# Optimization experiments

Measured on AMD Instinct MI355X. Metric: run time of the kernel, lower is better.

## Reference

```python
import jax, jax.numpy as jnp
import numpy as np

NUM_EMBEDDINGS = 1024
EMBEDDING_DIM = 64
COMMITMENT_COST = 0.25


def setup_inputs() -> dict:
    key = jax.random.key(0)
    k1, k2 = jax.random.split(key)
    inputs = jax.random.normal(k1, (16, EMBEDDING_DIM, 64, 64), dtype=jnp.float32)
    # nn.Embedding weight init: uniform(-1/K, 1/K)
    emb = jax.random.uniform(
        k2, (NUM_EMBEDDINGS, EMBEDDING_DIM), dtype=jnp.float32,
        minval=-1.0 / NUM_EMBEDDINGS, maxval=1.0 / NUM_EMBEDDINGS)
    return {"inputs": inputs, "emb": emb}


def reference(inputs, emb):
    # NCHW -> NHWC
    x = jnp.transpose(inputs, (0, 2, 3, 1))  # [B,H,W,D]
    B, H, W, D = x.shape
    K = emb.shape[0]
    flat = x.reshape(-1, D)  # [N,D]

    # squared L2 distances to every codebook entry: [N,K]
    distances = (jnp.sum(flat * flat, axis=1, keepdims=True)
                 + jnp.sum(emb * emb, axis=1)
                 - 2.0 * jnp.matmul(flat, emb.T))
    idx = jnp.argmin(distances, axis=1)  # [N]
    indices = idx.reshape(B, H, W)[:, None]  # [B,1,H,W]

    # gather == one-hot @ emb, but without the dense matmul
    quantized = emb[idx].reshape(B, H, W, D)

    e_latent_loss = jnp.mean((jax.lax.stop_gradient(quantized) - x) ** 2)
    q_latent_loss = jnp.mean((quantized - jax.lax.stop_gradient(x)) ** 2)
    loss = q_latent_loss + COMMITMENT_COST * e_latent_loss

    # straight-through estimator
    quantized_st = x + jax.lax.stop_gradient(quantized - x)

    # one-hot encodings are part of the module's return contract
    encodings = jax.nn.one_hot(idx, K, dtype=jnp.float32)  # [N,K]
    avg_probs = jnp.mean(encodings, axis=0)
    perplexity = jnp.exp(-jnp.sum(avg_probs * jnp.log(avg_probs + 1e-10)))

    quantized_out = jnp.transpose(quantized_st, (0, 3, 1, 2))  # back to NCHW
    return (loss, quantized_out, perplexity, encodings, indices)
```

## Files before the change

### kernel.cpp

```cpp
#include <hip/hip_runtime.h>

#define NPIX    65536
#define D       64
#define KCODES  1024
#define PIXB    32
#define BLOCK   256
#define XPAD    68
#define CAP     64
#define GFAC    0.036f

#define QUANT_OFF 1
#define PERP_OFF  4194305
#define ENC_OFF   4194306u
#define IDX_OFF   71303170u


typedef float f32x4 __attribute__((ext_vector_type(4)));
typedef short bf16x8 __attribute__((ext_vector_type(8)));

__device__ __forceinline__ unsigned short f2bf(float f) {
    unsigned u = __float_as_uint(f);
    return (unsigned short)((u + 0x7fffu + ((u >> 16) & 1u)) >> 16);
}

__global__ __launch_bounds__(256) void vq_init(const float* __restrict__ emb,
                                               double* __restrict__ loss_sum,
                                               int* __restrict__ counts,
                                               float* __restrict__ se,
                                               int* __restrict__ semax_bits,
                                               unsigned short* __restrict__ ebf) {
    int t = blockIdx.x * 256 + threadIdx.x;
    if (t == 0) *loss_sum = 0.0;
    if (t < KCODES) {
        counts[t] = 0;
        const float* e = emb + (size_t)t * D;
        float r[8];
        #pragma unroll
        for (int j = 0; j < 8; ++j) r[j] = __fmul_rn(e[j], e[j]);
        #pragma unroll
        for (int i = 8; i < D; i += 8)
            #pragma unroll
            for (int j = 0; j < 8; ++j)
                r[j] = __fadd_rn(r[j], __fmul_rn(e[i + j], e[i + j]));
        float X = __fadd_rn(__fadd_rn(r[0], r[1]), __fadd_rn(r[2], r[3]));
        float Y = __fadd_rn(__fadd_rn(r[4], r[5]), __fadd_rn(r[6], r[7]));
        float S = __fadd_rn(X, Y);
        se[t] = S;
        atomicMax(semax_bits, __float_as_int(S));
        #pragma unroll
        for (int j = 0; j < D; ++j) ebf[(t << 6) + j] = f2bf(e[j]);
    }
}

__global__ __launch_bounds__(256) void vq_main(const float* __restrict__ in,
                                               const float* __restrict__ emb,
                                               const float* __restrict__ se,
                                               const int* __restrict__ semax_bits,
                                               const unsigned short* __restrict__ ebf,
                                               float* __restrict__ out,
                                               double* __restrict__ loss_sum,
                                               int* __restrict__ counts) {
    __shared__ float xs[PIXB][XPAD];
    __shared__ float sls[KCODES];
    __shared__ float wmin[4][PIXB];
    __shared__ float gate[PIXB];
    __shared__ float sxs[PIXB];
    __shared__ int   cnt[PIXB];
    __shared__ int   skfin[PIXB];
    __shared__ unsigned short list[PIXB][CAP];

    const int tid  = threadIdx.x;
    const int lane = tid & 63;
    const int wid  = tid >> 6;
    const int n0   = blockIdx.x * PIXB;
    const int b    = n0 >> 12;
    const int s0   = n0 & 4095;

    {
        const float* base = in + ((size_t)b << 18) + s0;
        #pragma unroll
        for (int i = 0; i < 8; ++i) {
            int idx = tid + (i << 8);
            int d   = idx >> 5;
            int px  = idx & 31;
            xs[px][d] = base[((size_t)d << 12) + px];
        }
        #pragma unroll
        for (int i = 0; i < 4; ++i)
            sls[tid + (i << 8)] = se[tid + (i << 8)];
    }
    __syncthreads();

    if (tid < PIXB) {
        cnt[tid] = 0;
        float r[8];
        #pragma unroll
        for (int j = 0; j < 8; ++j) {
            float v = xs[tid][j];
            r[j] = __fmul_rn(v, v);
        }
        #pragma unroll
        for (int i = 8; i < D; i += 8)
            #pragma unroll
            for (int j = 0; j < 8; ++j) {
                float v = xs[tid][i + j];
                r[j] = __fadd_rn(r[j], __fmul_rn(v, v));
            }
        float X = __fadd_rn(__fadd_rn(r[0], r[1]), __fadd_rn(r[2], r[3]));
        float Y = __fadd_rn(__fadd_rn(r[4], r[5]), __fadd_rn(r[6], r[7]));
        sxs[tid] = __fadd_rn(X, Y);
    }

    const int wbase = wid * 256;
    const int arow  = lane & 15;
    const int kgrp  = (lane >> 4) << 3;
    const int rbase = (lane >> 4) << 2;

    bf16x8 af[2][2];
    #pragma unroll
    for (int ks = 0; ks < 2; ++ks)
        #pragma unroll
        for (int pt = 0; pt < 2; ++pt) {
            const float* xp = &xs[pt * 16 + arow][ks * 32 + kgrp];
            bf16x8 v;
            #pragma unroll
            for (int j = 0; j < 8; ++j) v[j] = (short)f2bf(xp[j]);
            af[ks][pt] = v;
        }

    float mreg[2][4];
    #pragma unroll
    for (int pt = 0; pt < 2; ++pt)
        #pragma unroll
        for (int r = 0; r < 4; ++r) mreg[pt][r] = 3.0e38f;

    #pragma unroll
    for (int s2 = 0; s2 < 8; ++s2) {
        const int cbase = wbase + s2 * 32;
        f32x4 acc[2][2];
        #pragma unroll
        for (int pt = 0; pt < 2; ++pt)
            #pragma unroll
            for (int kt = 0; kt < 2; ++kt) acc[pt][kt] = (f32x4){0.f, 0.f, 0.f, 0.f};
        #pragma unroll
        for (int ks = 0; ks < 2; ++ks)
            #pragma unroll
            for (int kt = 0; kt < 2; ++kt) {
                int code = cbase + kt * 16 + arow;
                bf16x8 bf_ = *(const bf16x8*)(ebf + ((size_t)code << 6) + ks * 32 + kgrp);
                #pragma unroll
                for (int pt = 0; pt < 2; ++pt)
                    acc[pt][kt] = __builtin_amdgcn_mfma_f32_16x16x32_bf16(
                        af[ks][pt], bf_, acc[pt][kt], 0, 0, 0);
            }
        #pragma unroll
        for (int pt = 0; pt < 2; ++pt)
            #pragma unroll
            for (int kt = 0; kt < 2; ++kt) {
                int code = cbase + kt * 16 + arow;
                #pragma unroll
                for (int r = 0; r < 4; ++r) {
                    float sv = __fsub_rn(sls[code], __fmul_rn(2.0f, acc[pt][kt][r]));
                    mreg[pt][r] = fminf(mreg[pt][r], sv);
                }
            }
    }
    #pragma unroll
    for (int m = 1; m < 16; m <<= 1)
        #pragma unroll
        for (int pt = 0; pt < 2; ++pt)
            #pragma unroll
            for (int r = 0; r < 4; ++r)
                mreg[pt][r] = fminf(mreg[pt][r], __shfl_xor(mreg[pt][r], m));
    if (arow == 0) {
        #pragma unroll
        for (int pt = 0; pt < 2; ++pt)
            #pragma unroll
            for (int r = 0; r < 4; ++r)
                wmin[wid][pt * 16 + rbase + r] = mreg[pt][r];
    }
    __syncthreads();

    if (tid < PIXB) {
        float gm = wmin[0][tid];
        #pragma unroll
        for (int w = 1; w < 4; ++w) gm = fminf(gm, wmin[w][tid]);
        float semax = __int_as_float(*semax_bits);
        gate[tid] = gm + GFAC * sqrtf(sxs[tid] * semax);
    }
    __syncthreads();

    #pragma unroll
    for (int s2 = 0; s2 < 8; ++s2) {
        const int cbase = wbase + s2 * 32;
        f32x4 acc[2][2];
        #pragma unroll
        for (int pt = 0; pt < 2; ++pt)
            #pragma unroll
            for (int kt = 0; kt < 2; ++kt) acc[pt][kt] = (f32x4){0.f, 0.f, 0.f, 0.f};
        #pragma unroll
        for (int ks = 0; ks < 2; ++ks)
            #pragma unroll
            for (int kt = 0; kt < 2; ++kt) {
                int code = cbase + kt * 16 + arow;
                bf16x8 bf_ = *(const bf16x8*)(ebf + ((size_t)code << 6) + ks * 32 + kgrp);
                #pragma unroll
                for (int pt = 0; pt < 2; ++pt)
                    acc[pt][kt] = __builtin_amdgcn_mfma_f32_16x16x32_bf16(
                        af[ks][pt], bf_, acc[pt][kt], 0, 0, 0);
            }
        #pragma unroll
        for (int pt = 0; pt < 2; ++pt)
            #pragma unroll
            for (int kt = 0; kt < 2; ++kt) {
                int code = cbase + kt * 16 + arow;
                #pragma unroll
                for (int r = 0; r < 4; ++r) {
                    float sv = __fsub_rn(sls[code], __fmul_rn(2.0f, acc[pt][kt][r]));
                    int px = pt * 16 + rbase + r;
                    if (sv <= gate[px]) {
                        int slot = atomicAdd(&cnt[px], 1);
                        if (slot < CAP) list[px][slot] = (unsigned short)code;
                    }
                }
            }
    }
    __syncthreads();

    {
        const int px = tid >> 3, c0 = tid & 7;
        const int cn = cnt[px];
        float bv = 3.0e38f;
        int   bk = 0x7fffffff;
        if (cn > CAP || cn == 0) {
            for (int k = c0; k < KCODES; k += 8) {
                const float* er = emb + ((size_t)k << 6);
                float m = 0.f;
                #pragma unroll
                for (int d = 0; d < D; ++d) m = fmaf(xs[px][d], er[d], m);
                float sv = __fsub_rn(__fadd_rn(sxs[px], sls[k]), __fmul_rn(2.0f, m));
                if (sv < bv || (sv == bv && k < bk)) { bv = sv; bk = k; }
            }
        } else {
            for (int i = c0; i < cn; i += 8) {
                int k = list[px][i];
                const float* er = emb + ((size_t)k << 6);
                float m = 0.f;
                #pragma unroll
                for (int d = 0; d < D; ++d) m = fmaf(xs[px][d], er[d], m);
                float sv = __fsub_rn(__fadd_rn(sxs[px], sls[k]), __fmul_rn(2.0f, m));
                if (sv < bv || (sv == bv && k < bk)) { bv = sv; bk = k; }
            }
        }
        #pragma unroll
        for (int m = 4; m; m >>= 1) {
            float ov = __shfl_xor(bv, m);
            int   ok = __shfl_xor(bk, m);
            if (ov < bv || (ov == bv && ok < bk)) { bv = ov; bk = ok; }
        }
        if (c0 == 0) {
            skfin[px] = bk;
            atomicAdd(&counts[bk], 1);
            out[IDX_OFF + (unsigned)(n0 + px)] = (float)bk;
        }
    }
    __syncthreads();

    {
        float* qbase = out + QUANT_OFF + ((size_t)b << 18) + s0;
        float mse = 0.f;
        #pragma unroll
        for (int i = 0; i < 8; ++i) {
            int idx = tid + (i << 8);
            int d   = idx >> 5;
            int px  = idx & 31;
            float q = emb[((size_t)skfin[px] << 6) + d];
            qbase[((size_t)d << 12) + px] = q;
            float df = q - xs[px][d];
            mse = fmaf(df, df, mse);
        }
        #pragma unroll
        for (int off = 32; off; off >>= 1) mse += __shfl_down(mse, off);
        if (lane == 0) atomicAdd(loss_sum, (double)mse);
    }

    {
        float4* dst4 = (float4*)(out + ENC_OFF + (size_t)n0 * KCODES + 2);
        for (int i = tid; i < 8191; i += BLOCK) {
            int flat = (i << 2) + 2;
            int r0 = flat >> 10;
            int r1 = (flat + 3) >> 10;
            int k0 = skfin[r0];
            int k1 = skfin[r1];
            int c  = flat & 1023;
            float4 v;
            v.x = (c == k0) ? 1.f : 0.f;
            v.y = (c + 1 == k0) ? 1.f : 0.f;
            v.z = (((flat + 2) & 1023) == k1) ? 1.f : 0.f;
            v.w = (((flat + 3) & 1023) == k1) ? 1.f : 0.f;
            dst4[i] = v;
        }
        if (tid == 0) {
            float2* dh = (float2*)(out + ENC_OFF + (size_t)n0 * KCODES);
            int kh = skfin[0];
            float2 h2; h2.x = (kh == 0) ? 1.f : 0.f; h2.y = (kh == 1) ? 1.f : 0.f;
            *dh = h2;
            float2* dt = (float2*)(out + ENC_OFF + (size_t)n0 * KCODES + 32766);
            int kt = skfin[31];
            float2 t2; t2.x = (kt == 1022) ? 1.f : 0.f; t2.y = (kt == 1023) ? 1.f : 0.f;
            *dt = t2;
        }
    }
}

__global__ __launch_bounds__(256) void vq_fin(const double* __restrict__ loss_sum,
                                              const int* __restrict__ counts,
                                              float* __restrict__ out) {
    __shared__ double red[256];
    int t = threadIdx.x;
    double ent = 0.0;
    for (int k = t; k < KCODES; k += 256) {
        double p = (double)counts[k] / 65536.0;
        ent -= p * log(p + 1e-10);
    }
    red[t] = ent;
    __syncthreads();
    for (int o = 128; o; o >>= 1) {
        if (t < o) red[t] += red[t + o];
        __syncthreads();
    }
    if (t == 0) {
        out[PERP_OFF] = (float)exp(red[0]);
        out[0] = (float)(1.25 * (*loss_sum) / 4194304.0);
    }
}

extern "C" void kernel_launch(void* const* d_in, const int* in_sizes, int n_in,
                              void* d_out, int out_size, void* d_ws, size_t ws_size,
                              hipStream_t stream) {
    const float* in  = (const float*)d_in[0];
    const float* emb = (const float*)d_in[1];
    float* out = (float*)d_out;

    double*         loss_sum   = (double*)d_ws;
    int*            counts     = (int*)((char*)d_ws + 8);
    float*          se         = (float*)((char*)d_ws + 4104);
    int*            semax_bits = (int*)((char*)d_ws + 8200);
    unsigned short* ebf        = (unsigned short*)((char*)d_ws + 8320);

    vq_init<<<4, 256, 0, stream>>>(emb, loss_sum, counts, se, semax_bits, ebf);
    vq_main<<<NPIX / PIXB, BLOCK, 0, stream>>>(in, emb, se, semax_bits, ebf,
                                               out, loss_sum, counts);
    vq_fin<<<1, 256, 0, stream>>>(loss_sum, counts, out);
}
```

Baseline: 189.6 us.

## Give each wavefront its own 16 pixels over all codes, removing block barriers

Work is repartitioned so each wave owns 16 pixels and scans the full 1024-code codebook, instead of four waves splitting the codebook across 32 shared pixels. This drops the cross-wave min reduction and the block-wide __syncthreads between the gate, candidate, rescore and output phases, leaving only compiler barriers. Blocks now cover 64 pixels, and the candidate list cap is halved. In exchange, each MFMA B-fragment load from the bf16 codebook is reused by fewer pixel tiles, so codebook traffic per pixel roughly doubles. The smaller cap also makes the full 1024-code fallback scan more likely.

```diff
diff --git a/kernel.cpp b/kernel.cpp
--- a/kernel.cpp
+++ b/kernel.cpp
@@ -3,10 +3,12 @@
 #define NPIX    65536
 #define D       64
 #define KCODES  1024
-#define PIXB    32
+#define PPW     16
+#define WPB     4
+#define PIXB    (PPW*WPB)
 #define BLOCK   256
 #define XPAD    68
-#define CAP     64
+#define CAP     32
 #define GFAC    0.036f
 
 #define QUANT_OFF 1
@@ -60,30 +62,28 @@
                                                float* __restrict__ out,
                                                double* __restrict__ loss_sum,
                                                int* __restrict__ counts) {
-    __shared__ float xs[PIXB][XPAD];
+    __shared__ float xsw[WPB][PPW][XPAD];
     __shared__ float sls[KCODES];
-    __shared__ float wmin[4][PIXB];
-    __shared__ float gate[PIXB];
-    __shared__ float sxs[PIXB];
-    __shared__ int   cnt[PIXB];
-    __shared__ int   skfin[PIXB];
-    __shared__ unsigned short list[PIXB][CAP];
+    __shared__ unsigned short listw[WPB][PPW][CAP];
+    __shared__ int   cntw[WPB][PPW];
+    __shared__ int   skw[WPB][PPW];
+    __shared__ float sxw[WPB][PPW];
 
     const int tid  = threadIdx.x;
     const int lane = tid & 63;
     const int wid  = tid >> 6;
-    const int n0   = blockIdx.x * PIXB;
-    const int b    = n0 >> 12;
-    const int s0   = n0 & 4095;
-
-    {
-        const float* base = in + ((size_t)b << 18) + s0;
-        #pragma unroll
-        for (int i = 0; i < 8; ++i) {
-            int idx = tid + (i << 8);
-            int d   = idx >> 5;
-            int px  = idx & 31;
-            xs[px][d] = base[((size_t)d << 12) + px];
+    const int c0   = lane & 15;
+    const int grp  = lane >> 4;
+    const int n0w  = blockIdx.x * PIXB + wid * PPW;
+    const int b    = n0w >> 12;
+    const int s0w  = n0w & 4095;
+
+    {
+        const float* base = in + ((size_t)b << 18) + s0w;
+        #pragma unroll
+        for (int i = 0; i < 16; ++i) {
+            int d = i * 4 + grp;
+            xsw[wid][c0][d] = base[((size_t)d << 12) + c0];
         }
         #pragma unroll
         for (int i = 0; i < 4; ++i)
@@ -91,192 +91,135 @@
     }
     __syncthreads();
 
-    if (tid < PIXB) {
-        cnt[tid] = 0;
+    if (lane < PPW) {
+        cntw[wid][lane] = 0;
         float r[8];
         #pragma unroll
         for (int j = 0; j < 8; ++j) {
-            float v = xs[tid][j];
+            float v = xsw[wid][lane][j];
             r[j] = __fmul_rn(v, v);
         }
         #pragma unroll
         for (int i = 8; i < D; i += 8)
             #pragma unroll
             for (int j = 0; j < 8; ++j) {
-                float v = xs[tid][i + j];
+                float v = xsw[wid][lane][i + j];
                 r[j] = __fadd_rn(r[j], __fmul_rn(v, v));
             }
         float X = __fadd_rn(__fadd_rn(r[0], r[1]), __fadd_rn(r[2], r[3]));
         float Y = __fadd_rn(__fadd_rn(r[4], r[5]), __fadd_rn(r[6], r[7]));
-        sxs[tid] = __fadd_rn(X, Y);
-    }
-
-    const int wbase = wid * 256;
-    const int arow  = lane & 15;
-    const int kgrp  = (lane >> 4) << 3;
-    const int rbase = (lane >> 4) << 2;
-
-    bf16x8 af[2][2];
+        sxw[wid][lane] = __fadd_rn(X, Y);
+    }
+
+    bf16x8 af[2];
     #pragma unroll
-    for (int ks = 0; ks < 2; ++ks)
-        #pragma unroll
-        for (int pt = 0; pt < 2; ++pt) {
-            const float* xp = &xs[pt * 16 + arow][ks * 32 + kgrp];
-            bf16x8 v;
-            #pragma unroll
-            for (int j = 0; j < 8; ++j) v[j] = (short)f2bf(xp[j]);
-            af[ks][pt] = v;
-        }
-
-    float mreg[2][4];
+    for (int ks = 0; ks < 2; ++ks) {
+        const float* xp = &xsw[wid][c0][ks * 32 + (grp << 3)];
+        bf16x8 v;
+        #pragma unroll
+        for (int j = 0; j < 8; ++j) v[j] = (short)f2bf(xp[j]);
+        af[ks] = v;
+    }
+    const float semax = __int_as_float(*semax_bits);
+
+    float m[4] = {3.0e38f, 3.0e38f, 3.0e38f, 3.0e38f};
+    for (int t = 0; t < 64; ++t) {
+        f32x4 acc = (f32x4){0.f, 0.f, 0.f, 0.f};
+        #pragma unroll
+        for (int ks = 0; ks < 2; ++ks) {
+            bf16x8 bf_ = *(const bf16x8*)(ebf + ((size_t)((t << 4) + c0) << 6)
+                                          + ks * 32 + (grp << 3));
+            acc = __builtin_amdgcn_mfma_f32_16x16x32_bf16(af[ks], bf_, acc, 0, 0, 0);
+        }
+        float sl = sls[(t << 4) + c0];
+        #pragma unroll
+        for (int r = 0; r < 4; ++r) {
+            float sv = __fsub_rn(sl, __fmul_rn(2.0f, acc[r]));
+            m[r] = fminf(m[r], sv);
+        }
+    }
     #pragma unroll
-    for (int pt = 0; pt < 2; ++pt)
-        #pragma unroll
-        for (int r = 0; r < 4; ++r) mreg[pt][r] = 3.0e38f;
-
+    for (int msk = 1; msk < 16; msk <<= 1)
+        #pragma unroll
+        for (int r = 0; r < 4; ++r)
+            m[r] = fminf(m[r], __shfl_xor(m[r], msk));
+
+    float gate[4];
     #pragma unroll
-    for (int s2 = 0; s2 < 8; ++s2) {
-        const int cbase = wbase + s2 * 32;
-        f32x4 acc[2][2];
-        #pragma unroll
-        for (int pt = 0; pt < 2; ++pt)
-            #pragma unroll
-            for (int kt = 0; kt < 2; ++kt) acc[pt][kt] = (f32x4){0.f, 0.f, 0.f, 0.f};
-        #pragma unroll
-        for (int ks = 0; ks < 2; ++ks)
-            #pragma unroll
-            for (int kt = 0; kt < 2; ++kt) {
-                int code = cbase + kt * 16 + arow;
-                bf16x8 bf_ = *(const bf16x8*)(ebf + ((size_t)code << 6) + ks * 32 + kgrp);
-                #pragma unroll
-                for (int pt = 0; pt < 2; ++pt)
-                    acc[pt][kt] = __builtin_amdgcn_mfma_f32_16x16x32_bf16(
-                        af[ks][pt], bf_, acc[pt][kt], 0, 0, 0);
-            }
-        #pragma unroll
-        for (int pt = 0; pt < 2; ++pt)
-            #pragma unroll
-            for (int kt = 0; kt < 2; ++kt) {
-                int code = cbase + kt * 16 + arow;
-                #pragma unroll
-                for (int r = 0; r < 4; ++r) {
-                    float sv = __fsub_rn(sls[code], __fmul_rn(2.0f, acc[pt][kt][r]));
-                    mreg[pt][r] = fminf(mreg[pt][r], sv);
-                }
-            }
-    }
-    #pragma unroll
-    for (int m = 1; m < 16; m <<= 1)
-        #pragma unroll
-        for (int pt = 0; pt < 2; ++pt)
-            #pragma unroll
-            for (int r = 0; r < 4; ++r)
-                mreg[pt][r] = fminf(mreg[pt][r], __shfl_xor(mreg[pt][r], m));
-    if (arow == 0) {
-        #pragma unroll
-        for (int pt = 0; pt < 2; ++pt)
-            #pragma unroll
-            for (int r = 0; r < 4; ++r)
-                wmin[wid][pt * 16 + rbase + r] = mreg[pt][r];
-    }
-    __syncthreads();
-
-    if (tid < PIXB) {
-        float gm = wmin[0][tid];
-        #pragma unroll
-        for (int w = 1; w < 4; ++w) gm = fminf(gm, wmin[w][tid]);
-        float semax = __int_as_float(*semax_bits);
-        gate[tid] = gm + GFAC * sqrtf(sxs[tid] * semax);
-    }
-    __syncthreads();
-
-    #pragma unroll
-    for (int s2 = 0; s2 < 8; ++s2) {
-        const int cbase = wbase + s2 * 32;
-        f32x4 acc[2][2];
-        #pragma unroll
-        for (int pt = 0; pt < 2; ++pt)
-            #pragma unroll
-            for (int kt = 0; kt < 2; ++kt) acc[pt][kt] = (f32x4){0.f, 0.f, 0.f, 0.f};
-        #pragma unroll
-        for (int ks = 0; ks < 2; ++ks)
-            #pragma unroll
-            for (int kt = 0; kt < 2; ++kt) {
-                int code = cbase + kt * 16 + arow;
-                bf16x8 bf_ = *(const bf16x8*)(ebf + ((size_t)code << 6) + ks * 32 + kgrp);
-                #pragma unroll
-                for (int pt = 0; pt < 2; ++pt)
-                    acc[pt][kt] = __builtin_amdgcn_mfma_f32_16x16x32_bf16(
-                        af[ks][pt], bf_, acc[pt][kt], 0, 0, 0);
-            }
-        #pragma unroll
-        for (int pt = 0; pt < 2; ++pt)
-            #pragma unroll
-            for (int kt = 0; kt < 2; ++kt) {
-                int code = cbase + kt * 16 + arow;
-                #pragma unroll
-                for (int r = 0; r < 4; ++r) {
-                    float sv = __fsub_rn(sls[code], __fmul_rn(2.0f, acc[pt][kt][r]));
-                    int px = pt * 16 + rbase + r;
-                    if (sv <= gate[px]) {
-                        int slot = atomicAdd(&cnt[px], 1);
-                        if (slot < CAP) list[px][slot] = (unsigned short)code;
-                    }
-                }
-            }
-    }
-    __syncthreads();
-
-    {
-        const int px = tid >> 3, c0 = tid & 7;
-        const int cn = cnt[px];
+    for (int r = 0; r < 4; ++r)
+        gate[r] = m[r] + GFAC * sqrtf(sxw[wid][(grp << 2) + r] * semax);
+    asm volatile("" ::: "memory");
+
+    for (int t = 0; t < 64; ++t) {
+        f32x4 acc = (f32x4){0.f, 0.f, 0.f, 0.f};
+        #pragma unroll
+        for (int ks = 0; ks < 2; ++ks) {
+            bf16x8 bf_ = *(const bf16x8*)(ebf + ((size_t)((t << 4) + c0) << 6)
+                                          + ks * 32 + (grp << 3));
+            acc = __builtin_amdgcn_mfma_f32_16x16x32_bf16(af[ks], bf_, acc, 0, 0, 0);
+        }
+        float sl = sls[(t << 4) + c0];
+        #pragma unroll
+        for (int r = 0; r < 4; ++r) {
+            float sv = __fsub_rn(sl, __fmul_rn(2.0f, acc[r]));
+            if (sv <= gate[r]) {
+                int px = (grp << 2) + r;
+                int slot = atomicAdd(&cntw[wid][px], 1);
+                if (slot < CAP) listw[wid][px][slot] = (unsigned short)((t << 4) + c0);
+            }
+        }
+    }
+    asm volatile("" ::: "memory");
+
+    {
+        const int px = c0, sub = grp;
+        const int cn = cntw[wid][px];
         float bv = 3.0e38f;
         int   bk = 0x7fffffff;
         if (cn > CAP || cn == 0) {
-            for (int k = c0; k < KCODES; k += 8) {
+            for (int k = sub; k < KCODES; k += 4) {
                 const float* er = emb + ((size_t)k << 6);
-                float m = 0.f;
+                float mm = 0.f;
                 #pragma unroll
-                for (int d = 0; d < D; ++d) m = fmaf(xs[px][d], er[d], m);
-                float sv = __fsub_rn(__fadd_rn(sxs[px], sls[k]), __fmul_rn(2.0f, m));
+                for (int d = 0; d < D; ++d) mm = fmaf(xsw[wid][px][d], er[d], mm);
+                float sv = __fsub_rn(__fadd_rn(sxw[wid][px], sls[k]), __fmul_rn(2.0f, mm));
                 if (sv < bv || (sv == bv && k < bk)) { bv = sv; bk = k; }
             }
         } else {
-            for (int i = c0; i < cn; i += 8) {
-                int k = list[px][i];
+            for (int i = sub; i < cn; i += 4) {
+                int k = listw[wid][px][i];
                 const float* er = emb + ((size_t)k << 6);
-                float m = 0.f;
+                float mm = 0.f;
                 #pragma unroll
-                for (int d = 0; d < D; ++d) m = fmaf(xs[px][d], er[d], m);
-                float sv = __fsub_rn(__fadd_rn(sxs[px], sls[k]), __fmul_rn(2.0f, m));
+                for (int d = 0; d < D; ++d) mm = fmaf(xsw[wid][px][d], er[d], mm);
+                float sv = __fsub_rn(__fadd_rn(sxw[wid][px], sls[k]), __fmul_rn(2.0f, mm));
                 if (sv < bv || (sv == bv && k < bk)) { bv = sv; bk = k; }
             }
         }
         #pragma unroll
-        for (int m = 4; m; m >>= 1) {
-            float ov = __shfl_xor(bv, m);
-            int   ok = __shfl_xor(bk, m);
+        for (int msk = 16; msk < 64; msk <<= 1) {
+            float ov = __shfl_xor(bv, msk);
+            int   ok = __shfl_xor(bk, msk);
             if (ov < bv || (ov == bv && ok < bk)) { bv = ov; bk = ok; }
         }
-        if (c0 == 0) {
-            skfin[px] = bk;
+        if (sub == 0) {
+            skw[wid][px] = bk;
             atomicAdd(&counts[bk], 1);
-            out[IDX_OFF + (unsigned)(n0 + px)] = (float)bk;
-        }
-    }
-    __syncthreads();
-
-    {
-        float* qbase = out + QUANT_OFF + ((size_t)b << 18) + s0;
+            out[IDX_OFF + (unsigned)(n0w + px)] = (float)bk;
+        }
+    }
+    asm volatile("" ::: "memory");
+
+    {
+        float* qbase = out + QUANT_OFF + ((size_t)b << 18) + s0w;
+        const float* eq = emb + ((size_t)skw[wid][c0] << 6);
         float mse = 0.f;
         #pragma unroll
-        for (int i = 0; i < 8; ++i) {
-            int idx = tid + (i << 8);
-            int d   = idx >> 5;
-            int px  = idx & 31;
-            float q = emb[((size_t)skfin[px] << 6) + d];
-            qbase[((size_t)d << 12) + px] = q;
-            float df = q - xs[px][d];
+        for (int i = 0; i < 16; ++i) {
+            int d = i * 4 + grp;
+            float q = eq[d];
+            qbase[((size_t)d << 12) + c0] = q;
+            float df = q - xsw[wid][c0][d];
             mse = fmaf(df, df, mse);
         }
         #pragma unroll
@@ -285,13 +228,13 @@
     }
 
     {
-        float4* dst4 = (float4*)(out + ENC_OFF + (size_t)n0 * KCODES + 2);
-        for (int i = tid; i < 8191; i += BLOCK) {
+        float4* dst4 = (float4*)(out + ENC_OFF + (size_t)n0w * KCODES + 2);
+        for (int i = lane; i < 4095; i += 64) {
             int flat = (i << 2) + 2;
             int r0 = flat >> 10;
             int r1 = (flat + 3) >> 10;
-            int k0 = skfin[r0];
-            int k1 = skfin[r1];
+            int k0 = skw[wid][r0];
+            int k1 = skw[wid][r1];
             int c  = flat & 1023;
             float4 v;
             v.x = (c == k0) ? 1.f : 0.f;
@@ -300,13 +243,13 @@
             v.w = (((flat + 3) & 1023) == k1) ? 1.f : 0.f;
             dst4[i] = v;
         }
-        if (tid == 0) {
-            float2* dh = (float2*)(out + ENC_OFF + (size_t)n0 * KCODES);
-            int kh = skfin[0];
+        if (lane == 0) {
+            float2* dh = (float2*)(out + ENC_OFF + (size_t)n0w * KCODES);
+            int kh = skw[wid][0];
             float2 h2; h2.x = (kh == 0) ? 1.f : 0.f; h2.y = (kh == 1) ? 1.f : 0.f;
             *dh = h2;
-            float2* dt = (float2*)(out + ENC_OFF + (size_t)n0 * KCODES + 32766);
-            int kt = skfin[31];
+            float2* dt = (float2*)(out + ENC_OFF + (size_t)n0w * KCODES + 16382);
+            int kt = skw[wid][15];
             float2 t2; t2.x = (kt == 1022) ? 1.f : 0.f; t2.y = (kt == 1023) ? 1.f : 0.f;
             *dt = t2;
         }
```

New measurement: 215.6 us. +13.7%, slower.
